# Kernel optimization log

Hardware: AMD Instinct MI355X
Metric: run time of the kernel (lower is better)

Reference implementation:

```python
import jax, jax.numpy as jnp
import numpy as np
import math

BS, QLEN, DIM, NHEADS = 2, 2048, 1024, 16
DPH = DIM // NHEADS


def setup_inputs() -> dict:
    key = jax.random.key(0)
    ks = jax.random.split(key, 10)
    s = 0.02
    return {
        "input": jax.random.normal(ks[0], (BS, QLEN, DIM), jnp.float32),
        "mask": jax.random.randint(ks[1], (BS, QLEN), 0, 2, jnp.int32),
        "Wq": jax.random.normal(ks[2], (DIM, DIM), jnp.float32) * s,
        "bq": jnp.zeros((DIM,), jnp.float32),
        "Wk": jax.random.normal(ks[3], (DIM, DIM), jnp.float32) * s,
        "bk": jnp.zeros((DIM,), jnp.float32),
        "Wv": jax.random.normal(ks[4], (DIM, DIM), jnp.float32) * s,
        "bv": jnp.zeros((DIM,), jnp.float32),
        "Wo": jax.random.normal(ks[5], (DIM, DIM), jnp.float32) * s,
        "bo": jnp.zeros((DIM,), jnp.float32),
    }


def _shape(x):
    # (bs, len, dim) -> (bs, heads, len, dph)
    return x.reshape(BS, -1, NHEADS, DPH).transpose(0, 2, 1, 3)


def reference(input, mask, Wq, bq, Wk, bk, Wv, bv, Wo, bo):
    q = _shape(input @ Wq.T + bq)
    k = _shape(input @ Wk.T + bk)
    v = _shape(input @ Wv.T + bv)
    q = q / math.sqrt(DPH)
    scores = jnp.einsum("bhqd,bhkd->bhqk", q, k)  # (bs, h, qlen, klen)
    # original masked_fill_ with 1e-10 (NOT -inf)
    m = (mask == 0)[:, None, None, :]  # (bs,1,1,klen)
    scores = jnp.where(m, jnp.float32(1e-10), scores)
    weights = jax.nn.softmax(scores.astype(jnp.float32), axis=-1).astype(scores.dtype)
    # dropout p=0.0 / eval mode -> identity
    context = jnp.einsum("bhqk,bhkd->bhqd", weights, v)
    context = context.transpose(0, 2, 1, 3).reshape(BS, -1, DIM)
    return context @ Wo.T + bo
```

## Files before the change

### kernel.cpp

```cpp
#include <hip/hip_runtime.h>

typedef __attribute__((ext_vector_type(8))) _Float16 half8;
typedef __attribute__((ext_vector_type(4))) _Float16 half4;
typedef __attribute__((ext_vector_type(4))) float f32x4;
typedef __attribute__((ext_vector_type(16))) float f32x16;
typedef __attribute__((ext_vector_type(4))) int int4v;

#define BS 2
#define QLEN 2048
#define DIM 1024
#define NH 16
#define DPH 64
#define MTOT (BS * QLEN)
#define LOG2E 1.44269504088896340736f

__global__ void cvt_all(const float* __restrict__ x,
                        const float* __restrict__ wq, const float* __restrict__ wk,
                        const float* __restrict__ wv, const float* __restrict__ wo,
                        _Float16* __restrict__ X16,
                        _Float16* __restrict__ Wq16, _Float16* __restrict__ Wk16,
                        _Float16* __restrict__ Wv16, _Float16* __restrict__ Wo16) {
    const int NX = (MTOT * DIM) / 4;
    const int NW = (DIM * DIM) / 4;
    const int total = NX + 4 * NW;
    int idx = blockIdx.x * blockDim.x + threadIdx.x;
    int stride = gridDim.x * blockDim.x;
    for (int i = idx; i < total; i += stride) {
        const float* src; _Float16* dst; int off;
        if (i < NX) { src = x; dst = X16; off = i; }
        else {
            int k = i - NX; int which = k / NW; off = k - which * NW;
            src = which == 0 ? wq : which == 1 ? wk : which == 2 ? wv : wo;
            dst = which == 0 ? Wq16 : which == 1 ? Wk16 : which == 2 ? Wv16 : Wo16;
        }
        float4 v = ((const float4*)src)[off];
        half4 o;
        o[0] = (_Float16)v.x; o[1] = (_Float16)v.y;
        o[2] = (_Float16)v.z; o[3] = (_Float16)v.w;
        ((half4*)dst)[off] = o;
    }
}

__device__ __forceinline__ void gload_lds16(const _Float16* g, _Float16* l) {
    __builtin_amdgcn_global_load_lds(
        (const __attribute__((address_space(1))) void*)g,
        (__attribute__((address_space(3))) void*)l, 16, 0, 0);
}

__global__ __launch_bounds__(256) void gemm_qkv(
    const _Float16* __restrict__ A,
    const _Float16* __restrict__ Wq, const _Float16* __restrict__ Wk,
    const _Float16* __restrict__ Wv,
    const float* __restrict__ bq, const float* __restrict__ bk,
    const float* __restrict__ bv, const int* __restrict__ mask,
    _Float16* __restrict__ Qd, _Float16* __restrict__ Kd,
    _Float16* __restrict__ Vd) {
    const int K = 1024;
    __shared__ _Float16 sA[2][128 * 32];
    __shared__ _Float16 sB[2][128 * 32];

    const int flat = blockIdx.x;
    const int xcd = flat & 7, seq = flat >> 3;
    const int ya = xcd >> 1, nb = xcd & 1;
    const int n_hi = seq & 3;
    const int rem = seq >> 2;
    const int z = rem % 3, y_hi = rem / 3;
    const int y = y_hi * 4 + ya;
    const int nblk = n_hi * 2 + nb;
    const int m0 = y * 128, n0 = nblk * 128;

    const _Float16* W = (z == 0) ? Wq : (z == 1) ? Wk : Wv;
    const float* bias = (z == 0) ? bq : (z == 1) ? bk : bv;

    const int tid = threadIdx.x, w = tid >> 6, l = tid & 63;
    const int wr = (w >> 1) * 64, wc = (w & 1) * 64;
    const int r = l & 15, g = l >> 4;

    const _Float16* gA[2];
    const _Float16* gW[2];
    _Float16* dA[2];
    _Float16* dB[2];
#pragma unroll
    for (int i = 0; i < 2; ++i) {
        int s = tid + i * 256, row = s >> 2, pos = s & 3;
        int chunk = pos ^ (row & 3);
        gA[i] = &A[(size_t)(m0 + row) * K + chunk * 8];
        gW[i] = &W[(size_t)(n0 + row) * K + chunk * 8];
        dA[i] = &sA[0][s * 8];
        dB[i] = &sB[0][s * 8];
    }
    auto stageAdv = [&](int bb) {
#pragma unroll
        for (int i = 0; i < 2; ++i) {
            gload_lds16(gA[i], dA[i] + bb * 4096);
            gload_lds16(gW[i], dB[i] + bb * 4096);
            gA[i] += 32;
            gW[i] += 32;
        }
    };

    const int fpos = (g ^ (r & 3)) * 8;
    const _Float16* pA[4];
    const _Float16* pB[4];
#pragma unroll
    for (int i = 0; i < 4; ++i) {
        pA[i] = &sA[0][(wr + i * 16 + r) * 32] + fpos;
        pB[i] = &sB[0][(wc + i * 16 + r) * 32] + fpos;
    }

    f32x4 acc[4][4] = {};
    auto compute = [&](int bb) {
        const int boff = bb * 4096;
        half8 af[4], bf[4];
#pragma unroll
        for (int i = 0; i < 4; ++i) {
            af[i] = *(const half8*)(pA[i] + boff);
            bf[i] = *(const half8*)(pB[i] + boff);
        }
#pragma unroll
        for (int i = 0; i < 4; ++i)
#pragma unroll
            for (int j = 0; j < 4; ++j)
                acc[i][j] = __builtin_amdgcn_mfma_f32_16x16x32_f16(
                    af[i], bf[j], acc[i][j], 0, 0, 0);
    };

    stageAdv(0);
    __syncthreads();
    for (int t = 0; t < 16; ++t) {
        stageAdv(1);
        compute(0);
        __syncthreads();
        stageAdv(0);
        compute(1);
        __syncthreads();
    }

    float bv4[4];
#pragma unroll
    for (int j = 0; j < 4; ++j) bv4[j] = bias[n0 + wc + j * 16 + r];

#pragma unroll
    for (int i = 0; i < 4; ++i)
#pragma unroll
        for (int j = 0; j < 4; ++j) {
            const int n = n0 + wc + j * 16 + r;
            const int h = n >> 6, d = n & 63;
#pragma unroll
            for (int reg = 0; reg < 4; ++reg) {
                const int m = m0 + wr + i * 16 + g * 4 + reg;
                const int bb = m >> 11, tt = m & 2047;
                float v = acc[i][j][reg] + bv4[j];
                if (z == 0)
                    Qd[(((size_t)(bb * NH + h)) * QLEN + tt) * DPH + d] =
                        (_Float16)(v * (0.125f * LOG2E));
                else if (z == 1) {
                    v = mask[bb * QLEN + tt] ? v : 0.f;
                    Kd[(((size_t)(bb * NH + h)) * QLEN + tt) * DPH + d] = (_Float16)v;
                } else
                    Vd[(((size_t)(bb * NH + h)) * DPH + d) * QLEN + tt] = (_Float16)v;
            }
        }
}

__global__ __launch_bounds__(256) void gemm_out(
    const _Float16* __restrict__ A, const _Float16* __restrict__ W,
    const float* __restrict__ bias, float* __restrict__ out) {
    const int K = 1024;
    __shared__ _Float16 sA[2][64 * 32];
    __shared__ _Float16 sB[2][128 * 32];
    const int m0 = blockIdx.y * 64, n0 = blockIdx.x * 128;
    const int tid = threadIdx.x, w = tid >> 6, l = tid & 63;
    const int wr = (w >> 1) * 32, wc = (w & 1) * 64;
    const int r = l & 15, g = l >> 4;

    auto stage = [&](int k0, int bb) {
        {
            int c = tid;
            int row = c >> 2, seg = (c & 3) * 8;
            gload_lds16(&A[(size_t)(m0 + row) * K + k0 + seg], &sA[bb][c * 8]);
        }
#pragma unroll
        for (int i = 0; i < 2; ++i) {
            int c = tid + i * 256;
            int row = c >> 2, seg = (c & 3) * 8;
            gload_lds16(&W[(size_t)(n0 + row) * K + k0 + seg], &sB[bb][c * 8]);
        }
    };

    f32x4 acc[2][4] = {};

    stage(0, 0);
    __syncthreads();
    int buf = 0;
    for (int k0 = 0; k0 < K; k0 += 32) {
        if (k0 + 32 < K) stage(k0 + 32, buf ^ 1);

        half8 af[2], bf[4];
#pragma unroll
        for (int i = 0; i < 2; ++i)
            af[i] = *(const half8*)&sA[buf][(wr + i * 16 + r) * 32 + g * 8];
#pragma unroll
        for (int j = 0; j < 4; ++j)
            bf[j] = *(const half8*)&sB[buf][(wc + j * 16 + r) * 32 + g * 8];
#pragma unroll
        for (int i = 0; i < 2; ++i)
#pragma unroll
            for (int j = 0; j < 4; ++j)
                acc[i][j] = __builtin_amdgcn_mfma_f32_16x16x32_f16(
                    af[i], bf[j], acc[i][j], 0, 0, 0);
        __syncthreads();
        buf ^= 1;
    }

    float bv4[4];
#pragma unroll
    for (int j = 0; j < 4; ++j) bv4[j] = bias[n0 + wc + j * 16 + r];
#pragma unroll
    for (int i = 0; i < 2; ++i)
#pragma unroll
        for (int j = 0; j < 4; ++j) {
            const int n = n0 + wc + j * 16 + r;
#pragma unroll
            for (int reg = 0; reg < 4; ++reg) {
                const int m = m0 + wr + i * 16 + g * 4 + reg;
                out[(size_t)m * DIM + n] = acc[i][j][reg] + bv4[j];
            }
        }
}

__global__ __launch_bounds__(512) void attn_kernel(
    const _Float16* __restrict__ Qg, const _Float16* __restrict__ Kg,
    const _Float16* __restrict__ Vg, _Float16* __restrict__ ctx) {
    __shared__ __align__(16) char smem[65536];

    const int flat = blockIdx.x;
    const int qt = (flat >> 3) & 15;
    const int bh = ((flat >> 7) << 3) | (flat & 7);
    const int b = bh >> 4, h = bh & 15;
    const _Float16* __restrict__ Qp = Qg + (size_t)bh * QLEN * DPH;
    const _Float16* __restrict__ Kp = Kg + (size_t)bh * QLEN * DPH;
    const _Float16* __restrict__ Vp = Vg + (size_t)bh * DPH * QLEN;

    const int tid = threadIdx.x, w = tid >> 6, l = tid & 63;
    const int qsub = w & 3, ksplit = w >> 2;
    const int ln = l & 31, hi = l >> 5;
    const int q0 = qt * 128 + qsub * 32;
    const int kbase = ksplit * 1024;

    _Float16* sK0 = (_Float16*)(smem + ksplit * 2 * 8192);
    _Float16* sV0 = (_Float16*)(smem + 32768 + ksplit * 2 * 8192);

    half8 qf[4];
#pragma unroll
    for (int ks = 0; ks < 4; ++ks)
        qf[ks] = *(const half8*)&Qp[(size_t)(q0 + ln) * DPH + ks * 16 + hi * 8];

    f32x16 accT[2] = {};
    float lsum = 0.f;

    const _Float16* kptr[2][4];
    const _Float16* vptr[2][2][2];
#pragma unroll
    for (int kb = 0; kb < 2; ++kb) {
#pragma unroll
        for (int ks = 0; ks < 4; ++ks)
            kptr[kb][ks] = sK0 + (kb * 32 + ln) * 64 + ((ks * 2 + hi) ^ (ln & 7)) * 8;
#pragma unroll
        for (int dblk = 0; dblk < 2; ++dblk) {
            vptr[kb][dblk][0] =
                sV0 + (dblk * 32 + ln) * 64 + ((kb * 4 + 0 + hi) ^ (ln & 7)) * 8;
            vptr[kb][dblk][1] =
                sV0 + (dblk * 32 + ln) * 64 + ((kb * 4 + 2 + hi) ^ (ln & 7)) * 8;
        }
    }

    const int c8 = ((l & 7) ^ (l >> 3)) * 8;
    const int rl = l >> 3;
    const _Float16* gK[2];
    const _Float16* gV[2];
    _Float16* dK[2];
    _Float16* dV[2];
#pragma unroll
    for (int j = 0; j < 2; ++j) {
        const int r0 = qsub * 16 + j * 8;
        gK[j] = &Kp[(size_t)(kbase + r0 + rl) * DPH + c8];
        gV[j] = &Vp[(size_t)(r0 + rl) * QLEN + kbase + c8];
        dK[j] = sK0 + r0 * 64 + l * 8;
        dV[j] = sV0 + r0 * 64 + l * 8;
    }

    auto stageAdv = [&](int bb) {
#pragma unroll
        for (int j = 0; j < 2; ++j) {
            gload_lds16(gK[j], dK[j] + bb * 4096);
            gload_lds16(gV[j], dV[j] + bb * 4096);
            gK[j] += 64 * DPH;
            gV[j] += 64;
        }
    };

    auto compute = [&](int bb) {
        const int boff = bb * 4096;
#pragma unroll
        for (int kb = 0; kb < 2; ++kb) {
            f32x16 st = {};
            __builtin_amdgcn_s_setprio(1);
#pragma unroll
            for (int ks = 0; ks < 4; ++ks) {
                half8 kf = *(const half8*)(kptr[kb][ks] + boff);
                st = __builtin_amdgcn_mfma_f32_32x32x16_f16(kf, qf[ks], st, 0, 0, 0);
            }
            __builtin_amdgcn_s_setprio(0);

            int cpk[8];
#pragma unroll
            for (int i = 0; i < 8; ++i) {
                float e0 = __builtin_amdgcn_exp2f(st[2 * i]);
                float e1 = __builtin_amdgcn_exp2f(st[2 * i + 1]);
                lsum += e0 + e1;
                cpk[i] =
                    __builtin_bit_cast(int, __builtin_amdgcn_cvt_pkrtz(e0, e1));
            }
            asm("v_permlane32_swap_b32 %0, %1" : "+v"(cpk[0]), "+v"(cpk[2]));
            asm("v_permlane32_swap_b32 %0, %1" : "+v"(cpk[1]), "+v"(cpk[3]));
            asm("v_permlane32_swap_b32 %0, %1" : "+v"(cpk[4]), "+v"(cpk[6]));
            asm("v_permlane32_swap_b32 %0, %1" : "+v"(cpk[5]), "+v"(cpk[7]));
            int4v b0 = {cpk[0], cpk[1], cpk[2], cpk[3]};
            int4v b1 = {cpk[4], cpk[5], cpk[6], cpk[7]};
            half8 Bf0 = __builtin_bit_cast(half8, b0);
            half8 Bf1 = __builtin_bit_cast(half8, b1);

            __builtin_amdgcn_s_setprio(1);
#pragma unroll
            for (int dblk = 0; dblk < 2; ++dblk) {
                half8 vf0 = *(const half8*)(vptr[kb][dblk][0] + boff);
                half8 vf1 = *(const half8*)(vptr[kb][dblk][1] + boff);
                accT[dblk] = __builtin_amdgcn_mfma_f32_32x32x16_f16(
                    vf0, Bf0, accT[dblk], 0, 0, 0);
                accT[dblk] = __builtin_amdgcn_mfma_f32_32x32x16_f16(
                    vf1, Bf1, accT[dblk], 0, 0, 0);
            }
            __builtin_amdgcn_s_setprio(0);
        }
    };

    stageAdv(0);
    __syncthreads();
    for (int t = 0; t < 8; ++t) {
        stageAdv(1);
        compute(0);
        __syncthreads();
        stageAdv(0);
        compute(1);
        __syncthreads();
    }

    lsum += __shfl_xor(lsum, 32);

    float* sRed = (float*)smem;
    if (ksplit == 1) {
        float* p = sRed + (qsub * 64 + l) * 33;
#pragma unroll
        for (int dblk = 0; dblk < 2; ++dblk)
#pragma unroll
            for (int i = 0; i < 16; ++i)
                p[dblk * 16 + i] = accT[dblk][i];
        p[32] = lsum;
    }
    __syncthreads();
    if (ksplit == 1) return;

    const float* p = sRed + (qsub * 64 + l) * 33;
#pragma unroll
    for (int dblk = 0; dblk < 2; ++dblk)
#pragma unroll
        for (int i = 0; i < 16; ++i)
            accT[dblk][i] += p[dblk * 16 + i];
    lsum += p[32];

    const float inv = 1.f / lsum;
    _Float16* cp = ctx + ((size_t)(b * QLEN) + q0 + ln) * DIM + h * DPH;
#pragma unroll
    for (int dblk = 0; dblk < 2; ++dblk)
#pragma unroll
        for (int j = 0; j < 4; ++j) {
            half4 o4;
#pragma unroll
            for (int e = 0; e < 4; ++e)
                o4[e] = (_Float16)(accT[dblk][4 * j + e] * inv);
            *(half4*)&cp[dblk * 32 + 8 * j + 4 * hi] = o4;
        }
}

extern "C" void kernel_launch(void* const* d_in, const int* in_sizes, int n_in,
                              void* d_out, int out_size, void* d_ws, size_t ws_size,
                              hipStream_t stream) {
    const float* x  = (const float*)d_in[0];
    const int* mask = (const int*)d_in[1];
    const float* Wq = (const float*)d_in[2];
    const float* bq = (const float*)d_in[3];
    const float* Wk = (const float*)d_in[4];
    const float* bk = (const float*)d_in[5];
    const float* Wv = (const float*)d_in[6];
    const float* bv = (const float*)d_in[7];
    const float* Wo = (const float*)d_in[8];
    const float* bo = (const float*)d_in[9];
    float* out = (float*)d_out;

    char* ws = (char*)d_ws;
    const size_t MB = 1u << 20;
    _Float16* X16  = (_Float16*)(ws + 0);
    _Float16* Wq16 = (_Float16*)(ws + 8 * MB);
    _Float16* Wk16 = (_Float16*)(ws + 10 * MB);
    _Float16* Wv16 = (_Float16*)(ws + 12 * MB);
    _Float16* Wo16 = (_Float16*)(ws + 14 * MB);
    _Float16* Q16  = (_Float16*)(ws + 16 * MB);
    _Float16* K16  = (_Float16*)(ws + 24 * MB);
    _Float16* V16T = (_Float16*)(ws + 32 * MB);
    _Float16* CTX  = (_Float16*)(ws + 40 * MB);

    cvt_all<<<2048, 256, 0, stream>>>(x, Wq, Wk, Wv, Wo,
                                      X16, Wq16, Wk16, Wv16, Wo16);

    gemm_qkv<<<768, 256, 0, stream>>>(
        X16, Wq16, Wk16, Wv16, bq, bk, bv, mask, Q16, K16, V16T);

    attn_kernel<<<512, 512, 0, stream>>>(Q16, K16, V16T, CTX);

    gemm_out<<<dim3(8, 64), 256, 0, stream>>>(CTX, Wo16, bo, out);
}
```

Measured before the change: 122.1 us.

## Replace full syncthreads with partial vmcnt waits in GEMM pipelines

Both the QKV GEMM and the output GEMM now wait with s_waitcnt vmcnt(N) before their barriers, so only the older LDS-bound loads must finish while the next stage's loads stay in flight. The output GEMM is also restructured to use precomputed advancing global and LDS pointers, with a fixed two-stage unrolled loop. Sched barriers pin instruction ordering. This aims to overlap global-to-LDS loads with MFMA compute and cut address arithmetic, at the risk of races if the vmcnt counts are wrong. The final iteration also issues an extra out-of-range prefetch.

Result: faster. 119.1 us (-2.4%).

```diff
diff --git a/kernel.cpp b/kernel.cpp
--- a/kernel.cpp
+++ b/kernel.cpp
@@ -13,6 +13,14 @@
 #define DPH 64
 #define MTOT (BS * QLEN)
 #define LOG2E 1.44269504088896340736f
+
+#define WAITB(N)                                          \
+    asm volatile("s_waitcnt vmcnt(" #N ")" ::: "memory"); \
+    __builtin_amdgcn_s_barrier();                         \
+    __builtin_amdgcn_sched_barrier(0)
+#define ENDB()                                            \
+    __builtin_amdgcn_sched_barrier(0);                    \
+    __builtin_amdgcn_s_barrier()
 
 __global__ void cvt_all(const float* __restrict__ x,
                         const float* __restrict__ wq, const float* __restrict__ wk,
@@ -126,14 +134,15 @@
     };
 
     stageAdv(0);
-    __syncthreads();
     for (int t = 0; t < 16; ++t) {
         stageAdv(1);
+        WAITB(4);
         compute(0);
-        __syncthreads();
+        ENDB();
         stageAdv(0);
+        WAITB(4);
         compute(1);
-        __syncthreads();
+        ENDB();
     }
 
     float bv4[4];
@@ -174,43 +183,67 @@
     const int wr = (w >> 1) * 32, wc = (w & 1) * 64;
     const int r = l & 15, g = l >> 4;
 
-    auto stage = [&](int k0, int bb) {
-        {
-            int c = tid;
-            int row = c >> 2, seg = (c & 3) * 8;
-            gload_lds16(&A[(size_t)(m0 + row) * K + k0 + seg], &sA[bb][c * 8]);
-        }
+    const _Float16* gA;
+    const _Float16* gB[2];
+    _Float16* dA;
+    _Float16* dB[2];
+    {
+        int s = tid, row = s >> 2, seg = (s & 3) * 8;
+        gA = &A[(size_t)(m0 + row) * K + seg];
+        dA = &sA[0][s * 8];
+    }
+#pragma unroll
+    for (int i = 0; i < 2; ++i) {
+        int s = tid + i * 256, row = s >> 2, seg = (s & 3) * 8;
+        gB[i] = &W[(size_t)(n0 + row) * K + seg];
+        dB[i] = &sB[0][s * 8];
+    }
+    auto stageAdv = [&](int bb) {
+        gload_lds16(gA, dA + bb * 2048);
+        gA += 32;
 #pragma unroll
         for (int i = 0; i < 2; ++i) {
-            int c = tid + i * 256;
-            int row = c >> 2, seg = (c & 3) * 8;
-            gload_lds16(&W[(size_t)(n0 + row) * K + k0 + seg], &sB[bb][c * 8]);
-        }
-    };
+            gload_lds16(gB[i], dB[i] + bb * 4096);
+            gB[i] += 32;
+        }
+    };
+
+    const _Float16* pA[2];
+    const _Float16* pB[4];
+#pragma unroll
+    for (int i = 0; i < 2; ++i)
+        pA[i] = &sA[0][(wr + i * 16 + r) * 32 + g * 8];
+#pragma unroll
+    for (int j = 0; j < 4; ++j)
+        pB[j] = &sB[0][(wc + j * 16 + r) * 32 + g * 8];
 
     f32x4 acc[2][4] = {};
-
-    stage(0, 0);
-    __syncthreads();
-    int buf = 0;
-    for (int k0 = 0; k0 < K; k0 += 32) {
-        if (k0 + 32 < K) stage(k0 + 32, buf ^ 1);
-
+    auto compute = [&](int bb) {
         half8 af[2], bf[4];
 #pragma unroll
         for (int i = 0; i < 2; ++i)
-            af[i] = *(const half8*)&sA[buf][(wr + i * 16 + r) * 32 + g * 8];
+            af[i] = *(const half8*)(pA[i] + bb * 2048);
 #pragma unroll
         for (int j = 0; j < 4; ++j)
-            bf[j] = *(const half8*)&sB[buf][(wc + j * 16 + r) * 32 + g * 8];
+            bf[j] = *(const half8*)(pB[j] + bb * 4096);
 #pragma unroll
         for (int i = 0; i < 2; ++i)
 #pragma unroll
             for (int j = 0; j < 4; ++j)
                 acc[i][j] = __builtin_amdgcn_mfma_f32_16x16x32_f16(
                     af[i], bf[j], acc[i][j], 0, 0, 0);
-        __syncthreads();
-        buf ^= 1;
+    };
+
+    stageAdv(0);
+    for (int t = 0; t < 16; ++t) {
+        stageAdv(1);
+        WAITB(3);
+        compute(0);
+        ENDB();
+        stageAdv(0);
+        WAITB(3);
+        compute(1);
+        ENDB();
     }
 
     float bv4[4];
```
